# Performance work log

Measured on AMD Instinct MI355X. Metric: run time of the kernel, lower is better.

The kernel has to match this reference:

```python
import jax, jax.numpy as jnp
import numpy as np
import math

B, S, D, H = 4, 4096, 1024, 128

def setup_inputs() -> dict:
    key = jax.random.key(0)
    ks = jax.random.split(key, 4)
    scale = 1.0 / math.sqrt(D)
    return {
        "inputs": jax.random.normal(ks[0], (B, S, D), dtype=jnp.float32),
        "Wk": jax.random.normal(ks[1], (H, D), dtype=jnp.float32) * scale,
        "bk": jnp.zeros((H,), dtype=jnp.float32),
        "Wq": jax.random.normal(ks[2], (H, D), dtype=jnp.float32) * scale,
        "bq": jnp.zeros((H,), dtype=jnp.float32),
        "Wv": jax.random.normal(ks[3], (H, D), dtype=jnp.float32) * scale,
        "bv": jnp.zeros((H,), dtype=jnp.float32),
        "padding_mask": jnp.ones((B, S), dtype=jnp.int32),
    }

def reference(inputs, Wk, bk, Wq, bq, Wv, bv, padding_mask):
    # Linear projections: [B,S,D] x [H,D]^T -> [B,S,H]
    k = jnp.einsum('bsd,hd->bsh', inputs, Wk) + bk
    q = jnp.einsum('bsd,hd->bsh', inputs, Wq) + bq
    v = jnp.einsum('bsd,hd->bsh', inputs, Wv) + bv
    # Scaled dot-product scores: [B,S,S]
    scores = jnp.einsum('bqh,bkh->bqk', q, k) / jnp.sqrt(jnp.float32(k.shape[-1]))
    # Mask out padded key positions (mask==0 -> -1e9), broadcast over query dim
    scores = jnp.where(padding_mask[:, None, :] == 0, jnp.float32(-1e9), scores)
    weights = jax.nn.softmax(scores, axis=-1)
    # Dropout is identity in eval mode (reference runs inference / training=False)
    out = jnp.einsum('bqk,bkh->bqh', weights, v)
    return out
```

## Files before the change

kernel.cpp:

```cpp
#include <hip/hip_runtime.h>
#include <cmath>

#define B_ 4
#define S_ 4096
#define D_ 1024
#define H_ 128
#define M_ (B_*S_)
#define NQT 32

typedef _Float16 half8 __attribute__((ext_vector_type(8)));
typedef _Float16 half4 __attribute__((ext_vector_type(4)));
typedef float f32x4 __attribute__((ext_vector_type(4)));
typedef float f32x16 __attribute__((ext_vector_type(16)));
typedef int i32x4 __attribute__((ext_vector_type(4)));

#define LOG2E 1.44269504088896340f

__device__ __forceinline__ void gload16(const void* g, void* l) {
    __builtin_amdgcn_global_load_lds(
        (const __attribute__((address_space(1))) unsigned int*)g,
        (__attribute__((address_space(3))) unsigned int*)l,
        16, 0, 0);
}

__global__ __launch_bounds__(256) void conv_w(
    const float* __restrict__ Wq, const float* __restrict__ Wk,
    const float* __restrict__ Wv, _Float16* __restrict__ wh)
{
    const int idx  = blockIdx.x * 256 + threadIdx.x;
    const int base = idx * 8;
    const int m    = base >> 17;
    const int off  = base & ((H_ * D_) - 1);
    const float* src = (m == 0 ? Wq : m == 1 ? Wk : Wv) + off;
    const float4 a = ((const float4*)src)[0];
    const float4 c = ((const float4*)src)[1];
    half8 h = { (_Float16)a.x, (_Float16)a.y, (_Float16)a.z, (_Float16)a.w,
                (_Float16)c.x, (_Float16)c.y, (_Float16)c.z, (_Float16)c.w };
    *(half8*)(wh + base) = h;
}

__global__ __launch_bounds__(256, 4) void proj_kernel(
    const float* __restrict__ x, const _Float16* __restrict__ wh,
    const float* __restrict__ bq, const float* __restrict__ bk,
    const float* __restrict__ bv,
    _Float16* __restrict__ qh, _Float16* __restrict__ kh,
    _Float16* __restrict__ vt)
{
    __shared__ _Float16 Xs[2][64][72];
    __shared__ _Float16 Ws2[128][64];

    const int t = threadIdx.x;
    const int yb = blockIdx.y;
    const float* __restrict__ bias = (yb == 0) ? bq : (yb == 1) ? bk : bv;
    const int m0 = blockIdx.x * 64;
    const int w = t >> 6, lane = t & 63;
    const int lg = lane >> 4, lr = lane & 15;

    f32x4 acc[8];
    #pragma unroll
    for (int i = 0; i < 8; ++i) acc[i] = f32x4{0.f, 0.f, 0.f, 0.f};

    const int xrow = t >> 2, xc = (t & 3) * 16;
    const float* xbase = x + (size_t)(m0 + xrow) * D_ + xc;

    int wbyte[4];
    #pragma unroll
    for (int i = 0; i < 4; ++i) {
        const int wrow = 32 * w + 8 * i + (lane >> 3);
        const int wblk = (lane & 7) ^ (lane >> 3);
        wbyte[i] = (wrow * D_ + wblk * 8) * 2;
    }
    const char* whb = (const char*)(wh + (size_t)yb * H_ * D_);

    float4 xfA[4], xfB[4];

#define WISSUE(KT)                                                            \
    {                                                                         \
        const char* wsrc = whb + (KT) * (64 * 2);                             \
        _Pragma("unroll")                                                     \
        for (int i = 0; i < 4; ++i)                                           \
            gload16(wsrc + wbyte[i], &Ws2[32 * w + 8 * i][0]);                \
    }
#define XISSUE(KT, XS)                                                        \
    {                                                                         \
        const float4* xs_ = (const float4*)(xbase + (KT) * 64);               \
        _Pragma("unroll") for (int i = 0; i < 4; ++i) XS[i] = xs_[i];         \
    }
#define XWRITE(XS, BUF)                                                       \
    {                                                                         \
        _Pragma("unroll") for (int i = 0; i < 4; ++i) {                       \
            half4 h = { (_Float16)XS[i].x, (_Float16)XS[i].y,                 \
                        (_Float16)XS[i].z, (_Float16)XS[i].w };               \
            *(half4*)&Xs[BUF][xrow][xc + 4 * i] = h;                          \
        }                                                                     \
    }
#define PMFMA(BUF)                                                            \
    {                                                                         \
        _Pragma("unroll") for (int kk = 0; kk < 2; ++kk) {                    \
            half8 a = *(const half8*)&Xs[BUF][w * 16 + lr][kk * 32 + 8 * lg]; \
            _Pragma("unroll") for (int ni = 0; ni < 8; ++ni) {                \
                half8 bfr = *(const half8*)&Ws2[ni * 16 + lr]                 \
                                [((4 * kk + lg) ^ (lr & 7)) * 8];             \
                acc[ni] = __builtin_amdgcn_mfma_f32_16x16x32_f16(a, bfr, acc[ni], 0, 0, 0); \
            }                                                                 \
        }                                                                     \
    }

    XISSUE(0, xfA)
    XISSUE(1, xfB)
    XWRITE(xfA, 0)
    WISSUE(0)
    __syncthreads();

    for (int kt = 0; kt < 16; kt += 2) {
        PMFMA(0)
        XWRITE(xfB, 1)
        if (kt + 2 < 16) XISSUE(kt + 2, xfA)
        __syncthreads();
        WISSUE(kt + 1)
        __syncthreads();
        PMFMA(1)
        if (kt + 2 < 16) {
            XWRITE(xfA, 0)
            if (kt + 3 < 16) XISSUE(kt + 3, xfB)
            __syncthreads();
            WISSUE(kt + 2)
            __syncthreads();
        }
    }
#undef WISSUE
#undef XISSUE
#undef XWRITE
#undef PMFMA

    const float qscale = 0.08838834764831845f * LOG2E;
    const int rowb = m0 + w * 16 + lg * 4;
    #pragma unroll
    for (int ni = 0; ni < 8; ++ni) {
        const int col = ni * 16 + lr;
        const float bval = bias[col];
        if (yb == 0) {
            #pragma unroll
            for (int r = 0; r < 4; ++r)
                qh[(size_t)(rowb + r) * H_ + col] = (_Float16)((acc[ni][r] + bval) * qscale);
        } else if (yb == 1) {
            #pragma unroll
            for (int r = 0; r < 4; ++r)
                kh[(size_t)(rowb + r) * H_ + col] = (_Float16)(acc[ni][r] + bval);
        } else {
            const int bb = rowb >> 12, s0 = rowb & (S_ - 1);
            half4 h;
            #pragma unroll
            for (int r = 0; r < 4; ++r) h[r] = (_Float16)(acc[ni][r] + bval);
            *(half4*)&vt[(size_t)bb * H_ * S_ + (size_t)col * S_ + s0] = h;
        }
    }
}

__device__ __forceinline__ void attn_tile32(
    const _Float16 (&Kb)[64][128], const _Float16 (&Vb)[128][64],
    const half8 (&qf)[8], f32x16 (&acc2)[4], float& m_, float& l_,
    int muse, int lane)
{
    const unsigned long long bz = __ballot(muse == 0);
    const int l31 = lane & 31, l7 = lane & 7, hi = lane >> 5;

    f32x16 sf[2];
    #pragma unroll
    for (int nb = 0; nb < 2; ++nb)
        #pragma unroll
        for (int r = 0; r < 16; ++r) sf[nb][r] = 0.f;
    #pragma unroll
    for (int kt = 0; kt < 8; ++kt) {
        #pragma unroll
        for (int nb = 0; nb < 2; ++nb) {
            half8 kb = *(const half8*)&Kb[nb * 32 + l31][((2 * kt + hi) ^ l7) * 8];
            sf[nb] = __builtin_amdgcn_mfma_f32_32x32x16_f16(kb, qf[kt], sf[nb], 0, 0, 0);
        }
    }
    if (bz) {
        #pragma unroll
        for (int nb = 0; nb < 2; ++nb)
            #pragma unroll
            for (int r = 0; r < 16; ++r) {
                const int kv = nb * 32 + (r & 3) + 8 * (r >> 2) + 4 * hi;
                if ((bz >> kv) & 1ull) sf[nb][r] = -3e9f;
            }
    }
    float tmax = sf[0][0];
    #pragma unroll
    for (int nb = 0; nb < 2; ++nb)
        #pragma unroll
        for (int r = 0; r < 16; ++r) tmax = fmaxf(tmax, sf[nb][r]);
    tmax = fmaxf(tmax, __shfl_xor(tmax, 32));
    if (!__all(tmax <= m_ + 8.f)) {
        const float mn  = fmaxf(m_, tmax);
        const float scl = exp2f(m_ - mn);
        m_ = mn; l_ *= scl;
        #pragma unroll
        for (int hb = 0; hb < 4; ++hb) acc2[hb] *= scl;
    }
    float rsum = 0.f;
    #pragma unroll
    for (int nb = 0; nb < 2; ++nb)
        #pragma unroll
        for (int r = 0; r < 16; ++r) {
            const float p = exp2f(sf[nb][r] - m_);
            sf[nb][r] = p;
            rsum += p;
        }
    rsum += __shfl_xor(rsum, 32);
    l_ += rsum;

    int pkw[2][8];
    #pragma unroll
    for (int nb = 0; nb < 2; ++nb)
        #pragma unroll
        for (int i = 0; i < 8; ++i) {
            auto h2 = __builtin_amdgcn_cvt_pkrtz(sf[nb][2 * i], sf[nb][2 * i + 1]);
            pkw[nb][i] = __builtin_bit_cast(int, h2);
        }
    #pragma unroll
    for (int nb = 0; nb < 2; ++nb)
        #pragma unroll
        for (int hf = 0; hf < 2; ++hf) {
            const int i0 = hf * 4;
            const int sA = hi ? pkw[nb][i0 + 0] : pkw[nb][i0 + 2];
            const int sB = hi ? pkw[nb][i0 + 1] : pkw[nb][i0 + 3];
            const int rA = __shfl_xor(sA, 32);
            const int rB = __shfl_xor(sB, 32);
            const int n0 = hi ? rA : pkw[nb][i0 + 0];
            const int n1 = hi ? rB : pkw[nb][i0 + 1];
            const int n2 = hi ? pkw[nb][i0 + 2] : rA;
            const int n3 = hi ? pkw[nb][i0 + 3] : rB;
            pkw[nb][i0 + 0] = n0; pkw[nb][i0 + 1] = n1;
            pkw[nb][i0 + 2] = n2; pkw[nb][i0 + 3] = n3;
        }
    #pragma unroll
    for (int s = 0; s < 4; ++s) {
        const int nb = s >> 1, hf = s & 1;
        const half8 pb = __builtin_bit_cast(half8,
            i32x4{ pkw[nb][hf * 4 + 0], pkw[nb][hf * 4 + 1],
                   pkw[nb][hf * 4 + 2], pkw[nb][hf * 4 + 3] });
        #pragma unroll
        for (int hb = 0; hb < 4; ++hb) {
            half8 vb = *(const half8*)&Vb[hb * 32 + l31][((2 * s + hi) ^ l7) * 8];
            acc2[hb] = __builtin_amdgcn_mfma_f32_32x32x16_f16(vb, pb, acc2[hb], 0, 0, 0);
        }
    }
}

__global__ __launch_bounds__(256, 2) void attn_kernel(
    const _Float16* __restrict__ qh, const _Float16* __restrict__ kh,
    const _Float16* __restrict__ vt, const int* __restrict__ mask,
    float* __restrict__ pout, float* __restrict__ pm, float* __restrict__ pl,
    const int nsplit)
{
    __shared__ _Float16 Ks[2][64][128];
    __shared__ _Float16 Vs[2][128][64];

    const int t = threadIdx.x;
    const int id = blockIdx.x;
    int qt, sp, b;
    const int ncombo = B_ * nsplit;
    if ((ncombo & 7) == 0) {
        const int per_xcd = ncombo >> 3;
        const int j = id >> 3;
        qt = j & (NQT - 1);
        const int combo = (id & 7) * per_xcd + (j >> 5);
        sp = combo % nsplit; b = combo / nsplit;
    } else {
        qt = id & (NQT - 1);
        const int rest = id >> 5;
        sp = rest % nsplit; b = rest / nsplit;
    }
    const int q0 = qt * 128;
    const int w = t >> 6, lane = t & 63;
    const int l31 = lane & 31, hi = lane >> 5;
    const int kvlen  = S_ / nsplit;
    const int iters  = kvlen >> 6;
    const int kvbase = sp * kvlen;

    int kbyte[4], vbyte[4];
    #pragma unroll
    for (int i = 0; i < 4; ++i) {
        const int krow = 16 * w + 4 * i + (lane >> 4);
        const int kblk = (lane & 15) ^ (krow & 7);
        kbyte[i] = (krow * H_ + kblk * 8) * 2;
        const int vrow = 32 * w + 8 * i + (lane >> 3);
        const int vblk = (lane & 7) ^ (lane >> 3);
        vbyte[i] = (vrow * S_ + vblk * 8) * 2;
    }
    const char* kbase_b = (const char*)(kh + (size_t)(b * S_ + kvbase) * H_);
    const char* vbase_b = (const char*)(vt + (size_t)b * H_ * S_ + kvbase);
    const char* mbase_b = (const char*)(mask + b * S_ + kvbase + lane);

#define ISSUE_TILE(IT, NB)                                                    \
    {                                                                         \
        const char* kb_t = kbase_b + (size_t)(IT) * (64 * H_ * 2);            \
        const char* vb_t = vbase_b + (size_t)(IT) * (64 * 2);                 \
        _Pragma("unroll")                                                     \
        for (int i = 0; i < 4; ++i)                                           \
            gload16(kb_t + kbyte[i], &Ks[NB][16 * w + 4 * i][0]);             \
        _Pragma("unroll")                                                     \
        for (int i = 0; i < 4; ++i)                                           \
            gload16(vb_t + vbyte[i], &Vs[NB][32 * w + 8 * i][0]);             \
    }

    half8 qf[8];
    {
        const _Float16* qp = qh + (size_t)(b * S_ + q0 + 32 * w + l31) * H_ + 8 * hi;
        #pragma unroll
        for (int kt = 0; kt < 8; ++kt) qf[kt] = *(const half8*)(qp + 16 * kt);
    }

    float m_ = -1e30f, l_ = 0.f;
    f32x16 acc2[4];
    #pragma unroll
    for (int hb = 0; hb < 4; ++hb)
        #pragma unroll
        for (int r = 0; r < 16; ++r) acc2[hb][r] = 0.f;

    ISSUE_TILE(0, 0)
    int mA = *(const int*)mbase_b;
    int mB = 0;
    __syncthreads();

    for (int it = 0; it < iters; it += 2) {
        if (it + 1 < iters) {
            ISSUE_TILE(it + 1, 1)
            mB = *(const int*)(mbase_b + (size_t)(it + 1) * 256);
        }
        attn_tile32(Ks[0], Vs[0], qf, acc2, m_, l_, mA, lane);
        __syncthreads();
        if (it + 2 < iters) {
            ISSUE_TILE(it + 2, 0)
            mA = *(const int*)(mbase_b + (size_t)(it + 2) * 256);
        }
        if (it + 1 < iters)
            attn_tile32(Ks[1], Vs[1], qf, acc2, m_, l_, mB, lane);
        __syncthreads();
    }
#undef ISSUE_TILE

    const int qrow = b * S_ + q0 + 32 * w + l31;
    float* op = pout + (size_t)(sp * M_ + qrow) * H_;
    #pragma unroll
    for (int hb = 0; hb < 4; ++hb)
        #pragma unroll
        for (int i = 0; i < 8; ++i) {
            const int h = hb * 32 + 2 * (i & 1) + 8 * (i >> 1) + 4 * hi;
            float2 v2 = make_float2(acc2[hb][2 * i], acc2[hb][2 * i + 1]);
            *(float2*)(op + h) = v2;
        }
    if (hi == 0) {
        pm[sp * M_ + qrow] = m_;
        pl[sp * M_ + qrow] = l_;
    }
}

__global__ __launch_bounds__(256) void combine_kernel(
    const float* __restrict__ pout, const float* __restrict__ pm,
    const float* __restrict__ pl, float* __restrict__ out, const int nsplit)
{
    const int idx = blockIdx.x * 256 + threadIdx.x;
    const int row = idx >> 5;
    const int c4  = (idx & 31) * 4;
    float M = -1e30f;
    for (int sp = 0; sp < nsplit; ++sp) M = fmaxf(M, pm[sp * M_ + row]);
    float Z = 0.f;
    f32x4 o = f32x4{0.f, 0.f, 0.f, 0.f};
    for (int sp = 0; sp < nsplit; ++sp) {
        const float wgt = exp2f(pm[sp * M_ + row] - M);
        Z += wgt * pl[sp * M_ + row];
        const f32x4 p = *(const f32x4*)&pout[(size_t)(sp * M_ + row) * H_ + c4];
        o += wgt * p;
    }
    const float inv = 1.f / Z;
    *(f32x4*)&out[(size_t)row * H_ + c4] = o * inv;
}

extern "C" void kernel_launch(void* const* d_in, const int* in_sizes, int n_in,
                              void* d_out, int out_size, void* d_ws, size_t ws_size,
                              hipStream_t stream)
{
    (void)in_sizes; (void)n_in; (void)out_size;
    const float* x  = (const float*)d_in[0];
    const float* Wk = (const float*)d_in[1];
    const float* bk = (const float*)d_in[2];
    const float* Wq = (const float*)d_in[3];
    const float* bq = (const float*)d_in[4];
    const float* Wv = (const float*)d_in[5];
    const float* bv = (const float*)d_in[6];
    const int* mask = (const int*)d_in[7];

    char* ws = (char*)d_ws;
    const size_t qkvBytes = (size_t)M_ * H_ * sizeof(_Float16);
    _Float16* qh = (_Float16*)ws;
    _Float16* kh = (_Float16*)(ws + qkvBytes);
    _Float16* vt = (_Float16*)(ws + 2 * qkvBytes);
    _Float16* wh = (_Float16*)(ws + 3 * qkvBytes);
    const size_t whBytes = (size_t)3 * H_ * D_ * sizeof(_Float16);
    char* rest = ws + 3 * qkvBytes + whBytes;

    int nsplit = 4;
    const size_t perSplit = (size_t)M_ * H_ * 4 + 2 * (size_t)M_ * 4;
    while (nsplit > 1 &&
           3 * qkvBytes + whBytes + (size_t)nsplit * perSplit > ws_size) nsplit >>= 1;

    float* pout = (float*)rest;
    float* pm   = (float*)(rest + (size_t)nsplit * M_ * H_ * 4);
    float* pl   = pm + (size_t)nsplit * M_;

    conv_w<<<dim3(3 * H_ * D_ / (256 * 8)), 256, 0, stream>>>(Wq, Wk, Wv, wh);
    proj_kernel<<<dim3(M_ / 64, 3), 256, 0, stream>>>(x, wh, bq, bk, bv, qh, kh, vt);
    attn_kernel<<<dim3(NQT * B_ * nsplit), 256, 0, stream>>>(qh, kh, vt, mask, pout, pm, pl, nsplit);
    combine_kernel<<<dim3(M_ * H_ / (256 * 4)), 256, 0, stream>>>(pout, pm, pl, (float*)d_out, nsplit);
}
```

Baseline: 103.1 us.

## Split KV across warps within block and combine in LDS, dropping combine kernel

Restructures attention so each block handles 32 query rows and its four warps each process a quarter of the KV sequence with private LDS tiles, then merges the partial softmax states through shared memory. This removes the global split-KV partial buffers and the separate combine kernel launch. Each warp now streams its own K/V, so K/V global traffic per query row rises, and the per-warp loop waits on its loads with no double buffering, so load latency is exposed.

```diff
diff --git a/kernel.cpp b/kernel.cpp
--- a/kernel.cpp
+++ b/kernel.cpp
@@ -6,7 +6,6 @@
 #define D_ 1024
 #define H_ 128
 #define M_ (B_*S_)
-#define NQT 32
 
 typedef _Float16 half8 __attribute__((ext_vector_type(8)));
 typedef _Float16 half4 __attribute__((ext_vector_type(4)));
@@ -157,41 +156,39 @@
     }
 }
 
-__device__ __forceinline__ void attn_tile32(
-    const _Float16 (&Kb)[64][128], const _Float16 (&Vb)[128][64],
+struct KvBufs { _Float16 K[4][32][128]; _Float16 V[4][128][32]; };
+union AttnU {
+    KvBufs s;
+    float accL[4][64][65];
+};
+
+__device__ __forceinline__ void attn_tile32s(
+    const _Float16 (&Kb)[32][128], const _Float16 (&Vb)[128][32],
     const half8 (&qf)[8], f32x16 (&acc2)[4], float& m_, float& l_,
     int muse, int lane)
 {
     const unsigned long long bz = __ballot(muse == 0);
-    const int l31 = lane & 31, l7 = lane & 7, hi = lane >> 5;
-
-    f32x16 sf[2];
-    #pragma unroll
-    for (int nb = 0; nb < 2; ++nb)
-        #pragma unroll
-        for (int r = 0; r < 16; ++r) sf[nb][r] = 0.f;
+    const int l31 = lane & 31, hi = lane >> 5;
+    const int l7 = l31 & 7, l3 = l31 & 3;
+
+    f32x16 sf;
+    #pragma unroll
+    for (int r = 0; r < 16; ++r) sf[r] = 0.f;
     #pragma unroll
     for (int kt = 0; kt < 8; ++kt) {
-        #pragma unroll
-        for (int nb = 0; nb < 2; ++nb) {
-            half8 kb = *(const half8*)&Kb[nb * 32 + l31][((2 * kt + hi) ^ l7) * 8];
-            sf[nb] = __builtin_amdgcn_mfma_f32_32x32x16_f16(kb, qf[kt], sf[nb], 0, 0, 0);
-        }
+        half8 kb = *(const half8*)&Kb[l31][((2 * kt + hi) ^ l7) * 8];
+        sf = __builtin_amdgcn_mfma_f32_32x32x16_f16(kb, qf[kt], sf, 0, 0, 0);
     }
     if (bz) {
         #pragma unroll
-        for (int nb = 0; nb < 2; ++nb)
-            #pragma unroll
-            for (int r = 0; r < 16; ++r) {
-                const int kv = nb * 32 + (r & 3) + 8 * (r >> 2) + 4 * hi;
-                if ((bz >> kv) & 1ull) sf[nb][r] = -3e9f;
-            }
-    }
-    float tmax = sf[0][0];
-    #pragma unroll
-    for (int nb = 0; nb < 2; ++nb)
-        #pragma unroll
-        for (int r = 0; r < 16; ++r) tmax = fmaxf(tmax, sf[nb][r]);
+        for (int r = 0; r < 16; ++r) {
+            const int kv = (r & 3) + 8 * (r >> 2) + 4 * hi;
+            if ((bz >> kv) & 1ull) sf[r] = -3e9f;
+        }
+    }
+    float tmax = sf[0];
+    #pragma unroll
+    for (int r = 1; r < 16; ++r) tmax = fmaxf(tmax, sf[r]);
     tmax = fmaxf(tmax, __shfl_xor(tmax, 32));
     if (!__all(tmax <= m_ + 8.f)) {
         const float mn  = fmaxf(m_, tmax);
@@ -202,49 +199,39 @@
     }
     float rsum = 0.f;
     #pragma unroll
-    for (int nb = 0; nb < 2; ++nb)
-        #pragma unroll
-        for (int r = 0; r < 16; ++r) {
-            const float p = exp2f(sf[nb][r] - m_);
-            sf[nb][r] = p;
-            rsum += p;
-        }
+    for (int r = 0; r < 16; ++r) {
+        const float p = exp2f(sf[r] - m_);
+        sf[r] = p;
+        rsum += p;
+    }
     rsum += __shfl_xor(rsum, 32);
     l_ += rsum;
 
-    int pkw[2][8];
-    #pragma unroll
-    for (int nb = 0; nb < 2; ++nb)
-        #pragma unroll
-        for (int i = 0; i < 8; ++i) {
-            auto h2 = __builtin_amdgcn_cvt_pkrtz(sf[nb][2 * i], sf[nb][2 * i + 1]);
-            pkw[nb][i] = __builtin_bit_cast(int, h2);
-        }
-    #pragma unroll
-    for (int nb = 0; nb < 2; ++nb)
-        #pragma unroll
-        for (int hf = 0; hf < 2; ++hf) {
-            const int i0 = hf * 4;
-            const int sA = hi ? pkw[nb][i0 + 0] : pkw[nb][i0 + 2];
-            const int sB = hi ? pkw[nb][i0 + 1] : pkw[nb][i0 + 3];
-            const int rA = __shfl_xor(sA, 32);
-            const int rB = __shfl_xor(sB, 32);
-            const int n0 = hi ? rA : pkw[nb][i0 + 0];
-            const int n1 = hi ? rB : pkw[nb][i0 + 1];
-            const int n2 = hi ? pkw[nb][i0 + 2] : rA;
-            const int n3 = hi ? pkw[nb][i0 + 3] : rB;
-            pkw[nb][i0 + 0] = n0; pkw[nb][i0 + 1] = n1;
-            pkw[nb][i0 + 2] = n2; pkw[nb][i0 + 3] = n3;
-        }
-    #pragma unroll
-    for (int s = 0; s < 4; ++s) {
-        const int nb = s >> 1, hf = s & 1;
-        const half8 pb = __builtin_bit_cast(half8,
-            i32x4{ pkw[nb][hf * 4 + 0], pkw[nb][hf * 4 + 1],
-                   pkw[nb][hf * 4 + 2], pkw[nb][hf * 4 + 3] });
+    int pkw[8];
+    #pragma unroll
+    for (int i = 0; i < 8; ++i) {
+        auto h2 = __builtin_amdgcn_cvt_pkrtz(sf[2 * i], sf[2 * i + 1]);
+        pkw[i] = __builtin_bit_cast(int, h2);
+    }
+    i32x4 pbi[2];
+    #pragma unroll
+    for (int s = 0; s < 2; ++s) {
+        const int i0 = 4 * s;
+        const int sA = hi ? pkw[i0 + 0] : pkw[i0 + 2];
+        const int sB = hi ? pkw[i0 + 1] : pkw[i0 + 3];
+        const int rA = __shfl_xor(sA, 32);
+        const int rB = __shfl_xor(sB, 32);
+        pbi[s][0] = hi ? rA : pkw[i0 + 0];
+        pbi[s][1] = hi ? rB : pkw[i0 + 1];
+        pbi[s][2] = hi ? pkw[i0 + 2] : rA;
+        pbi[s][3] = hi ? pkw[i0 + 3] : rB;
+    }
+    #pragma unroll
+    for (int s = 0; s < 2; ++s) {
+        const half8 pb = __builtin_bit_cast(half8, pbi[s]);
         #pragma unroll
         for (int hb = 0; hb < 4; ++hb) {
-            half8 vb = *(const half8*)&Vb[hb * 32 + l31][((2 * s + hi) ^ l7) * 8];
+            half8 vb = *(const half8*)&Vb[hb * 32 + l31][((2 * s + hi) ^ l3) * 8];
             acc2[hb] = __builtin_amdgcn_mfma_f32_32x32x16_f16(vb, pb, acc2[hb], 0, 0, 0);
         }
     }
@@ -253,63 +240,53 @@
 __global__ __launch_bounds__(256, 2) void attn_kernel(
     const _Float16* __restrict__ qh, const _Float16* __restrict__ kh,
     const _Float16* __restrict__ vt, const int* __restrict__ mask,
-    float* __restrict__ pout, float* __restrict__ pm, float* __restrict__ pl,
-    const int nsplit)
-{
-    __shared__ _Float16 Ks[2][64][128];
-    __shared__ _Float16 Vs[2][128][64];
+    float* __restrict__ out)
+{
+    __shared__ AttnU u;
+    __shared__ float mlm[4][64], mll[4][64];
 
     const int t = threadIdx.x;
     const int id = blockIdx.x;
-    int qt, sp, b;
-    const int ncombo = B_ * nsplit;
-    if ((ncombo & 7) == 0) {
-        const int per_xcd = ncombo >> 3;
-        const int j = id >> 3;
-        qt = j & (NQT - 1);
-        const int combo = (id & 7) * per_xcd + (j >> 5);
-        sp = combo % nsplit; b = combo / nsplit;
-    } else {
-        qt = id & (NQT - 1);
-        const int rest = id >> 5;
-        sp = rest % nsplit; b = rest / nsplit;
-    }
-    const int q0 = qt * 128;
+    const int xx = id & 7;
+    const int b  = xx >> 1;
+    const int qt = (xx & 1) * 64 + (id >> 3);
+    const int q0 = qt * 32;
     const int w = t >> 6, lane = t & 63;
     const int l31 = lane & 31, hi = lane >> 5;
-    const int kvlen  = S_ / nsplit;
-    const int iters  = kvlen >> 6;
-    const int kvbase = sp * kvlen;
-
-    int kbyte[4], vbyte[4];
-    #pragma unroll
-    for (int i = 0; i < 4; ++i) {
-        const int krow = 16 * w + 4 * i + (lane >> 4);
+    const int kvw0 = w * (S_ / 4);
+    const int iters = (S_ / 4) / 32;
+
+    int kbyte[8], vbyte[8];
+    #pragma unroll
+    for (int i = 0; i < 8; ++i) {
+        const int krow = 4 * i + (lane >> 4);
         const int kblk = (lane & 15) ^ (krow & 7);
         kbyte[i] = (krow * H_ + kblk * 8) * 2;
-        const int vrow = 32 * w + 8 * i + (lane >> 3);
-        const int vblk = (lane & 7) ^ (lane >> 3);
+        const int vrow = 16 * i + (lane >> 2);
+        const int vblk = (lane & 3) ^ (vrow & 3);
         vbyte[i] = (vrow * S_ + vblk * 8) * 2;
     }
-    const char* kbase_b = (const char*)(kh + (size_t)(b * S_ + kvbase) * H_);
-    const char* vbase_b = (const char*)(vt + (size_t)b * H_ * S_ + kvbase);
-    const char* mbase_b = (const char*)(mask + b * S_ + kvbase + lane);
-
-#define ISSUE_TILE(IT, NB)                                                    \
-    {                                                                         \
-        const char* kb_t = kbase_b + (size_t)(IT) * (64 * H_ * 2);            \
-        const char* vb_t = vbase_b + (size_t)(IT) * (64 * 2);                 \
+    const char* kbase_b = (const char*)(kh + (size_t)(b * S_ + kvw0) * H_);
+    const char* vbase_b = (const char*)(vt + (size_t)b * H_ * S_ + kvw0);
+    const int*  mbase   = mask + b * S_ + kvw0 + l31;
+
+#define ISSUE_TILE(IT)                                                        \
+    {                                                                         \
+        const char* kb_t = kbase_b + (size_t)(IT) * (32 * H_ * 2);            \
+        const char* vb_t = vbase_b + (size_t)(IT) * (32 * 2);                 \
         _Pragma("unroll")                                                     \
-        for (int i = 0; i < 4; ++i)                                           \
-            gload16(kb_t + kbyte[i], &Ks[NB][16 * w + 4 * i][0]);             \
+        for (int i = 0; i < 8; ++i)                                           \
+            gload16(kb_t + kbyte[i], &u.s.K[w][4 * i][0]);                    \
         _Pragma("unroll")                                                     \
-        for (int i = 0; i < 4; ++i)                                           \
-            gload16(vb_t + vbyte[i], &Vs[NB][32 * w + 8 * i][0]);             \
-    }
+        for (int i = 0; i < 8; ++i)                                           \
+            gload16(vb_t + vbyte[i], &u.s.V[w][16 * i][0]);                   \
+    }
+#define WLGKM asm volatile("s_waitcnt lgkmcnt(0)" ::: "memory")
+#define WVM   asm volatile("s_waitcnt vmcnt(0)"   ::: "memory")
 
     half8 qf[8];
     {
-        const _Float16* qp = qh + (size_t)(b * S_ + q0 + 32 * w + l31) * H_ + 8 * hi;
+        const _Float16* qp = qh + (size_t)(b * S_ + q0 + l31) * H_ + 8 * hi;
         #pragma unroll
         for (int kt = 0; kt < 8; ++kt) qf[kt] = *(const half8*)(qp + 16 * kt);
     }
@@ -321,70 +298,63 @@
         #pragma unroll
         for (int r = 0; r < 16; ++r) acc2[hb][r] = 0.f;
 
-    ISSUE_TILE(0, 0)
-    int mA = *(const int*)mbase_b;
-    int mB = 0;
+    ISSUE_TILE(0)
+    int mreg = mbase[0];
+    WVM;
+    for (int it = 0; it < iters; ++it) {
+        attn_tile32s(u.s.K[w], u.s.V[w], qf, acc2, m_, l_, mreg, lane);
+        if (it + 1 < iters) {
+            WLGKM;
+            ISSUE_TILE(it + 1)
+            mreg = mbase[(it + 1) * 32];
+            WVM;
+        }
+    }
+#undef ISSUE_TILE
+#undef WLGKM
+#undef WVM
+
     __syncthreads();
-
-    for (int it = 0; it < iters; it += 2) {
-        if (it + 1 < iters) {
-            ISSUE_TILE(it + 1, 1)
-            mB = *(const int*)(mbase_b + (size_t)(it + 1) * 256);
-        }
-        attn_tile32(Ks[0], Vs[0], qf, acc2, m_, l_, mA, lane);
-        __syncthreads();
-        if (it + 2 < iters) {
-            ISSUE_TILE(it + 2, 0)
-            mA = *(const int*)(mbase_b + (size_t)(it + 2) * 256);
-        }
-        if (it + 1 < iters)
-            attn_tile32(Ks[1], Vs[1], qf, acc2, m_, l_, mB, lane);
-        __syncthreads();
-    }
-#undef ISSUE_TILE
-
-    const int qrow = b * S_ + q0 + 32 * w + l31;
-    float* op = pout + (size_t)(sp * M_ + qrow) * H_;
+    mlm[w][lane] = m_;
+    mll[w][lane] = l_;
     #pragma unroll
     for (int hb = 0; hb < 4; ++hb)
         #pragma unroll
-        for (int i = 0; i < 8; ++i) {
-            const int h = hb * 32 + 2 * (i & 1) + 8 * (i >> 1) + 4 * hi;
-            float2 v2 = make_float2(acc2[hb][2 * i], acc2[hb][2 * i + 1]);
-            *(float2*)(op + h) = v2;
-        }
-    if (hi == 0) {
-        pm[sp * M_ + qrow] = m_;
-        pl[sp * M_ + qrow] = l_;
-    }
-}
-
-__global__ __launch_bounds__(256) void combine_kernel(
-    const float* __restrict__ pout, const float* __restrict__ pm,
-    const float* __restrict__ pl, float* __restrict__ out, const int nsplit)
-{
-    const int idx = blockIdx.x * 256 + threadIdx.x;
-    const int row = idx >> 5;
-    const int c4  = (idx & 31) * 4;
-    float M = -1e30f;
-    for (int sp = 0; sp < nsplit; ++sp) M = fmaxf(M, pm[sp * M_ + row]);
-    float Z = 0.f;
-    f32x4 o = f32x4{0.f, 0.f, 0.f, 0.f};
-    for (int sp = 0; sp < nsplit; ++sp) {
-        const float wgt = exp2f(pm[sp * M_ + row] - M);
-        Z += wgt * pl[sp * M_ + row];
-        const f32x4 p = *(const f32x4*)&pout[(size_t)(sp * M_ + row) * H_ + c4];
-        o += wgt * p;
+        for (int r = 0; r < 16; ++r)
+            u.accL[w][lane][hb * 16 + r] = acc2[hb][r];
+    __syncthreads();
+
+    float M = mlm[0][lane];
+    #pragma unroll
+    for (int wp = 1; wp < 4; ++wp) M = fmaxf(M, mlm[wp][lane]);
+    float sc[4], Z = 0.f;
+    #pragma unroll
+    for (int wp = 0; wp < 4; ++wp) {
+        sc[wp] = exp2f(mlm[wp][lane] - M);
+        Z += sc[wp] * mll[wp][lane];
     }
     const float inv = 1.f / Z;
-    *(f32x4*)&out[(size_t)row * H_ + c4] = o * inv;
+    float* op = out + (size_t)(b * S_ + q0 + l31) * H_;
+    #pragma unroll
+    for (int i = 0; i < 8; ++i) {
+        const int r0 = 2 * i;
+        float v0 = 0.f, v1 = 0.f;
+        #pragma unroll
+        for (int wp = 0; wp < 4; ++wp) {
+            v0 += sc[wp] * u.accL[wp][lane][w * 16 + r0];
+            v1 += sc[wp] * u.accL[wp][lane][w * 16 + r0 + 1];
+        }
+        const int h = 32 * w + 2 * (i & 1) + 8 * (i >> 1) + 4 * hi;
+        float2 v2 = make_float2(v0 * inv, v1 * inv);
+        *(float2*)(op + h) = v2;
+    }
 }
 
 extern "C" void kernel_launch(void* const* d_in, const int* in_sizes, int n_in,
                               void* d_out, int out_size, void* d_ws, size_t ws_size,
                               hipStream_t stream)
 {
-    (void)in_sizes; (void)n_in; (void)out_size;
+    (void)in_sizes; (void)n_in; (void)out_size; (void)ws_size;
     const float* x  = (const float*)d_in[0];
     const float* Wk = (const float*)d_in[1];
     const float* bk = (const float*)d_in[2];
@@ -400,20 +370,8 @@
     _Float16* kh = (_Float16*)(ws + qkvBytes);
     _Float16* vt = (_Float16*)(ws + 2 * qkvBytes);
     _Float16* wh = (_Float16*)(ws + 3 * qkvBytes);
-    const size_t whBytes = (size_t)3 * H_ * D_ * sizeof(_Float16);
-    char* rest = ws + 3 * qkvBytes + whBytes;
-
-    int nsplit = 4;
-    const size_t perSplit = (size_t)M_ * H_ * 4 + 2 * (size_t)M_ * 4;
-    while (nsplit > 1 &&
-           3 * qkvBytes + whBytes + (size_t)nsplit * perSplit > ws_size) nsplit >>= 1;
-
-    float* pout = (float*)rest;
-    float* pm   = (float*)(rest + (size_t)nsplit * M_ * H_ * 4);
-    float* pl   = pm + (size_t)nsplit * M_;
 
     conv_w<<<dim3(3 * H_ * D_ / (256 * 8)), 256, 0, stream>>>(Wq, Wk, Wv, wh);
     proj_kernel<<<dim3(M_ / 64, 3), 256, 0, stream>>>(x, wh, bq, bk, bv, qh, kh, vt);
-    attn_kernel<<<dim3(NQT * B_ * nsplit), 256, 0, stream>>>(qh, kh, vt, mask, pout, pm, pl, nsplit);
-    combine_kernel<<<dim3(M_ * H_ / (256 * 4)), 256, 0, stream>>>(pout, pm, pl, (float*)d_out, nsplit);
-}
+    attn_kernel<<<dim3(512), 256, 0, stream>>>(qh, kh, vt, mask, (float*)d_out);
+}
```

Result: slower. 105.3 us (+2.1%).
